# Kernel tuning notes

Measured on AMD Instinct MI355X. Metric: run time of the kernel, lower is better.

Reference implementation:

```python
import jax, jax.numpy as jnp
import numpy as np

N_USERS = 8192
D = 128
E = 262144        # known edges (nonzero_idx rows)
K = 131072        # static pad size for data-dependent candidate extraction
COS_THR = 0.3
TAU = 0.2


def setup_inputs() -> dict:
    key = jax.random.key(0)
    k1, k2, k3, k4 = jax.random.split(key, 4)
    user_emb = jax.random.normal(k1, (N_USERS, D), dtype=jnp.float32)
    nonzero_idx = jax.random.randint(k2, (E, 2), 0, N_USERS)
    W = jax.random.normal(k3, (2, 2 * D), dtype=jnp.float32) * 0.05  # mlp_s weight [2, 2*latent]
    b = jnp.zeros((2,), dtype=jnp.float32)                            # mlp_s bias
    gumbel_noise = jax.random.gumbel(k4, (E + K, 2), dtype=jnp.float32)
    return {"user_emb": user_emb, "W": W, "b": b,
            "gumbel_noise": gumbel_noise, "nonzero_idx": nonzero_idx}


def reference(user_emb, W, b, gumbel_noise, nonzero_idx):
    n = user_emb.shape[0]
    # ---- get_candidate_pair ----
    norm = jnp.linalg.norm(user_emb, axis=1, keepdims=True)
    u = user_emb / jnp.maximum(norm, 1e-12)          # F.normalize(dim=1)
    cos = u @ u.T                                    # [n, n]
    diag = jnp.arange(n)
    cos = cos.at[diag, diag].set(-1.0)               # fill_diagonal_(-1)
    cos = cos.at[nonzero_idx[:, 0], nonzero_idx[:, 1]].set(-1.0)
    mask = cos > COS_THR
    # static-size nonzero; padded slots point at (0,0) where cos == -1,
    # so they behave as invalid candidates (weight 0 downstream).
    ci, cj = jnp.nonzero(mask, size=K, fill_value=0)
    cand_vals = cos[ci, cj]                          # padded entries = -1
    cand_idx = jnp.stack([ci, cj], axis=1)           # [K, 2]

    # ---- forward ----
    pair_idx = jnp.concatenate([nonzero_idx, cand_idx], axis=0)   # [E+K, 2]
    u_emb = user_emb[pair_idx[:, 0]]
    v_emb = user_emb[pair_idx[:, 1]]
    concat_emb = jnp.concatenate([u_emb, v_emb], axis=1)          # [E+K, 2D]
    logits = concat_emb @ W.T + b                                 # [E+K, 2]

    # hard gumbel-softmax (straight-through)
    y_soft = jax.nn.softmax((logits + gumbel_noise) / TAU, axis=-1)
    y_hard = jax.nn.one_hot(jnp.argmax(y_soft, axis=-1), 2, dtype=y_soft.dtype)
    gumbel_output = y_hard + y_soft - jax.lax.stop_gradient(y_soft)
    gumbel_retain = gumbel_output[:, 0]                           # [E+K]

    # ---- get_edge_weight ----
    cand_w = jnp.maximum(cand_vals, 0.0)                          # masked_fill(<0, 0)
    weights = jnp.concatenate([jnp.ones((E,), dtype=cand_w.dtype), cand_w])
    w = gumbel_retain * weights                                   # [E+K]
    gumbel_01 = w
    gumbel_retain_w = jnp.concatenate([w[:, None], w[:, None]], axis=0)  # [2(E+K), 1]
    return gumbel_01, gumbel_retain_w, pair_idx
```

## Files before the change

kernel.cpp:

```cpp
#include <hip/hip_runtime.h>
#include <hip/hip_bf16.h>
#include <math.h>

#define N_USERS 8192
#define DIMS    128
#define EDGES   262144
#define KCAND   131072
#define NTOT    (EDGES + KCAND)
#define LISTCAP 131072
#define CAPB    512
#define NTILES  2080
#define COS_THR 0.3f
#define EPS_SEL 6e-3f
#define LOGIT_MARGIN 2e-3f
#define DEADKEY 0xFFFFFFFFu

typedef short bf16x8 __attribute__((ext_vector_type(8)));
typedef float f32x4  __attribute__((ext_vector_type(4)));


__global__ __launch_bounds__(256) void prep_k(const float* __restrict__ x,
                                              const float* __restrict__ W,
                                              const int* __restrict__ nz,
                                              float* __restrict__ un,
                                              unsigned short* __restrict__ u0,
                                              float4* __restrict__ P,
                                              unsigned* __restrict__ excl) {
  if (blockIdx.x < 32) {
#pragma clang fp contract(off)
    int i = blockIdx.x * 256 + threadIdx.x;
    const float* r = x + (size_t)i * DIMS;
    float a[8];
#pragma unroll
    for (int j = 0; j < 8; ++j) { float t = r[j]; a[j] = t * t; }
    for (int b8 = 8; b8 < DIMS; b8 += 8) {
#pragma unroll
      for (int j = 0; j < 8; ++j) { float t = r[b8 + j]; a[j] = a[j] + t * t; }
    }
    float s = ((a[0] + a[1]) + (a[2] + a[3])) + ((a[4] + a[5]) + (a[6] + a[7]));
    float n = (float)sqrt((double)s);
    n = fmaxf(n, 1e-12f);
    unsigned short* slab = u0 + (size_t)(i >> 7) * 16384 + (i & 127) * 8;
#pragma unroll
    for (int cq = 0; cq < 16; ++cq) {
      unsigned short tmp[8];
#pragma unroll
      for (int t = 0; t < 8; ++t) {
        float v = r[cq * 8 + t] / n;
        un[(size_t)i * DIMS + cq * 8 + t] = v;
        __hip_bfloat16 h = __float2bfloat16(v);
        tmp[t] = *(unsigned short*)&h;
      }
      *(uint4*)(slab + (size_t)cq * 1024) = *(uint4*)tmp;
    }
    float a0 = 0.f, b0 = 0.f, a1 = 0.f, b1 = 0.f;
    for (int k = 0; k < DIMS; ++k) {
      float t = r[k];
      a0 = fmaf(t, W[k], a0);
      b0 = fmaf(t, W[128 + k], b0);
      a1 = fmaf(t, W[256 + k], a1);
      b1 = fmaf(t, W[384 + k], b1);
    }
    P[i] = make_float4(a0, b0, a1, b1);
  } else {
    int t = (blockIdx.x - 32) * 256 + threadIdx.x;
    if (t < EDGES) {
      int i = nz[2 * t], j = nz[2 * t + 1];
      atomicOr(&excl[(size_t)i * 256 + (j >> 5)], 1u << (j & 31));
    }
  }
}

__global__ __launch_bounds__(512) void mfma_pass(const unsigned short* __restrict__ u0,
                                                 uint2* __restrict__ list,
                                                 int* __restrict__ gcount) {
  __shared__ __align__(16) unsigned short As[4][4][128][8];
  __shared__ __align__(16) unsigned short Bs[4][4][128][8];
  __shared__ uint2 svec[CAPB];
  __shared__ int lcnt, lbase;

  const int tid  = threadIdx.x;
  const int lane = tid & 63;
  const int wv   = tid >> 6;
  const int quad = lane >> 4;
  const int l15  = lane & 15;

  int rem = blockIdx.x, bi = 0;
  while (rem >= 64 - bi) { rem -= 64 - bi; ++bi; }
  const int bj = bi + rem;
  const int I0 = bi * 128, J0 = bj * 128;
  const int moff = (wv & 3) * 32, noff = (wv >> 2) * 64;

  if (tid == 0) lcnt = 0;

  const uint4* __restrict__ Aslab = (const uint4*)(u0 + (size_t)bi * 16384);
  const uint4* __restrict__ Bslab = (const uint4*)(u0 + (size_t)bj * 16384);
  uint4 pA[4], pB[4];
#pragma unroll
  for (int it = 0; it < 4; ++it) {
    pA[it] = Aslab[it * 512 + tid];
    pB[it] = Bslab[it * 512 + tid];
  }
#pragma unroll
  for (int it = 0; it < 4; ++it) {
    ((uint4*)As)[it * 512 + tid] = pA[it];
    ((uint4*)Bs)[it * 512 + tid] = pB[it];
  }
  __syncthreads();

  f32x4 acc[2][4];
#pragma unroll
  for (int mt = 0; mt < 2; ++mt)
#pragma unroll
    for (int nt = 0; nt < 4; ++nt)
#pragma unroll
      for (int g = 0; g < 4; ++g) acc[mt][nt][g] = 0.f;

#pragma unroll
  for (int kc = 0; kc < 4; ++kc) {
    bf16x8 af[2], bfr[4];
#pragma unroll
    for (int mt = 0; mt < 2; ++mt)
      af[mt] = *(const bf16x8*)&As[kc][quad][moff + mt * 16 + l15][0];
#pragma unroll
    for (int nt = 0; nt < 4; ++nt)
      bfr[nt] = *(const bf16x8*)&Bs[kc][quad][noff + nt * 16 + l15][0];
#pragma unroll
    for (int mt = 0; mt < 2; ++mt)
#pragma unroll
      for (int nt = 0; nt < 4; ++nt)
        acc[mt][nt] = __builtin_amdgcn_mfma_f32_16x16x32_bf16(
            af[mt], bfr[nt], acc[mt][nt], 0, 0, 0);
  }

#pragma unroll
  for (int mt = 0; mt < 2; ++mt)
#pragma unroll
    for (int nt = 0; nt < 4; ++nt)
#pragma unroll
      for (int g = 0; g < 4; ++g) {
        float v = acc[mt][nt][g];
        if (v > COS_THR - EPS_SEL) {
          int i = I0 + moff + mt * 16 + quad * 4 + g;
          int j = J0 + noff + nt * 16 + l15;
          if (j > i) {
            int idx = atomicAdd(&lcnt, 2);
            if (idx + 1 < CAPB) {
              svec[idx]     = make_uint2(((unsigned)i << 13) | j,
                                         __float_as_uint(v));
              svec[idx + 1] = make_uint2(((unsigned)j << 13) | i,
                                         __float_as_uint(v));
            }
          }
        }
      }

  __syncthreads();
  int n = min(lcnt, CAPB);
  if (tid == 0) lbase = atomicAdd(gcount, n);
  __syncthreads();
  int base = lbase;
  for (int t = tid; t < n; t += 512) {
    int o = base + t;
    if (o < LISTCAP) list[o] = svec[t];
  }
}

__global__ __launch_bounds__(256) void resolve_hist_k(const float* __restrict__ un,
                                                      const unsigned* __restrict__ excl,
                                                      uint2* __restrict__ list,
                                                      const int* __restrict__ gcount,
                                                      int* __restrict__ row_cnt) {
  int t = blockIdx.x * 256 + threadIdx.x;
  int n = min(*gcount, LISTCAP);
  if (t >= n) return;
  uint2 e = list[t];
  int i = e.x >> 13, j = e.x & 8191;
  unsigned word = excl[(size_t)i * 256 + (j >> 5)];
  bool alive = !(i == j || ((word >> (j & 31)) & 1u));
  float v = __uint_as_float(e.y);
  if (alive && v <= COS_THR + EPS_SEL) {
    const float* a = un + (size_t)i * DIMS;
    const float* b = un + (size_t)j * DIMS;
    float s = 0.f;
    for (int k = 0; k < DIMS; ++k) s = fmaf(a[k], b[k], s);
    alive = (s > COS_THR);
    if (alive) list[t] = make_uint2(e.x, __float_as_uint(s));
  }
  if (!alive) list[t] = make_uint2(DEADKEY, 0u);
  else        atomicAdd(&row_cnt[i], 1);
}

__global__ __launch_bounds__(256) void scan8k(const int* __restrict__ cnt,
                                              int* __restrict__ off) {
  __shared__ int sm[256];
  int t = threadIdx.x;
  int base = t * 32;
  int s = 0;
  for (int i = 0; i < 32; ++i) s += cnt[base + i];
  sm[t] = s;
  __syncthreads();
  int x = s;
  for (int d = 1; d < 256; d <<= 1) {
    int y = (t >= d) ? sm[t - d] : 0;
    __syncthreads();
    x += y;
    sm[t] = x;
    __syncthreads();
  }
  int run = x - s;
  for (int i = 0; i < 32; ++i) { off[base + i] = run; run += cnt[base + i]; }
  if (t == 255) off[N_USERS] = x;
}

__global__ __launch_bounds__(256) void scatter_pad_k(const uint2* __restrict__ list,
                                                     const int* __restrict__ gcount,
                                                     const int* __restrict__ row_off,
                                                     int* __restrict__ row_pos,
                                                     int* __restrict__ cand_i,
                                                     int* __restrict__ cand_j,
                                                     float* __restrict__ cand_v) {
  int t = blockIdx.x * 256 + threadIdx.x;
  int n = min(*gcount, LISTCAP);
  int M = row_off[N_USERS];
  if (t < n) {
    uint2 e = list[t];
    if (e.x != DEADKEY) {
      int i = e.x >> 13, j = e.x & 8191;
      int pos = row_off[i] + atomicAdd(&row_pos[i], 1);
      if (pos < KCAND) {
        cand_i[pos] = i;
        cand_j[pos] = j;
        cand_v[pos] = __uint_as_float(e.y);
      }
    }
  }
  if (t >= M && t < KCAND) { cand_i[t] = 0; cand_j[t] = 0; cand_v[t] = -1.0f; }
}

__global__ __launch_bounds__(256) void sortrow_k(const int* __restrict__ row_off,
                                                 const int* __restrict__ row_cnt,
                                                 int* __restrict__ cand_j,
                                                 float* __restrict__ cand_v) {
  int r = blockIdx.x * 256 + threadIdx.x;
  if (r >= N_USERS) return;
  int o = row_off[r], c = row_cnt[r];
  if (o + c > KCAND) c = max(0, KCAND - o);
  for (int a = 1; a < c; ++a) {
    int jv = cand_j[o + a];
    float vv = cand_v[o + a];
    int b = a - 1;
    while (b >= 0 && cand_j[o + b] > jv) {
      cand_j[o + b + 1] = cand_j[o + b];
      cand_v[o + b + 1] = cand_v[o + b];
      --b;
    }
    cand_j[o + b + 1] = jv;
    cand_v[o + b + 1] = vv;
  }
}

__global__ __launch_bounds__(256) void finalize_k(const float* __restrict__ ue,
                                                  const float* __restrict__ W,
                                                  const float* __restrict__ b,
                                                  const float* __restrict__ g,
                                                  const int* __restrict__ nz,
                                                  const int* __restrict__ cand_i,
                                                  const int* __restrict__ cand_j,
                                                  const float* __restrict__ cand_v,
                                                  const float4* __restrict__ P,
                                                  float* __restrict__ out) {
  int p = blockIdx.x * 256 + threadIdx.x;
  if (p >= NTOT) return;

  int i, j;
  float wgt;
  if (p < EDGES) {
    i = nz[2 * p];
    j = nz[2 * p + 1];
    wgt = 1.0f;
  } else {
    int q = p - EDGES;
    i = cand_i[q];
    j = cand_j[q];
    wgt = fmaxf(cand_v[q], 0.0f);
  }

  float4 Pi = P[i], Pj = P[j];
  float l0 = Pi.x + Pj.y + b[0];
  float l1 = Pi.z + Pj.w + b[1];
  float g0 = g[2 * p], g1 = g[2 * p + 1];
  float s0 = l0 + g0, s1 = l1 + g1;

  if (fabsf(s0 - s1) < LOGIT_MARGIN) {
    const float* ri = ue + (size_t)i * DIMS;
    const float* rj = ue + (size_t)j * DIMS;
    float e0 = 0.f, e1 = 0.f;
    for (int k = 0; k < DIMS; ++k) {
      e0 = fmaf(ri[k], W[k], e0);
      e1 = fmaf(ri[k], W[256 + k], e1);
    }
    for (int k = 0; k < DIMS; ++k) {
      e0 = fmaf(rj[k], W[128 + k], e0);
      e1 = fmaf(rj[k], W[384 + k], e1);
    }
    s0 = (e0 + b[0]) + g0;
    s1 = (e1 + b[1]) + g1;
  }

  float w = (s0 >= s1) ? wgt : 0.0f;

  out[p] = w;
  out[NTOT + p] = w;
  out[2 * NTOT + p] = w;
  out[3 * NTOT + 2 * p + 0] = (float)i;
  out[3 * NTOT + 2 * p + 1] = (float)j;
}

extern "C" void kernel_launch(void* const* d_in, const int* in_sizes, int n_in,
                              void* d_out, int out_size, void* d_ws, size_t ws_size,
                              hipStream_t stream) {
  (void)in_sizes; (void)n_in; (void)out_size; (void)ws_size;

  const float* user_emb = (const float*)d_in[0];
  const float* W        = (const float*)d_in[1];
  const float* b        = (const float*)d_in[2];
  const float* gnoise   = (const float*)d_in[3];
  const int*   nz       = (const int*)d_in[4];
  float* out = (float*)d_out;

  char* ws = (char*)d_ws;
  float*          un      = (float*)(ws + 0);
  unsigned short* u0      = (unsigned short*)(ws + (4u << 20));
  unsigned*       excl    = (unsigned*)(ws + (6u << 20));
  char*           zbase   = ws + (14u << 20);
  int*            gcount  = (int*)(zbase);
  int*            row_cnt = (int*)(zbase + 64);
  int*            row_pos = (int*)(zbase + 64 + 32768);
  int*            row_off = (int*)(ws + (14u << 20) + (96u << 10));
  uint2*          list    = (uint2*)(ws + (15u << 20));
  int*            cand_i  = (int*)(ws + (16u << 20));
  int*            cand_j  = (int*)(ws + (16u << 20) + (512u << 10));
  float*          cand_v  = (float*)(ws + (17u << 20));
  float4*         P       = (float4*)(ws + (17u << 20) + (512u << 10));

  hipMemsetAsync(excl, 0, (8u << 20) + (96u << 10), stream);

  prep_k<<<32 + EDGES / 256, 256, 0, stream>>>(user_emb, W, nz, un, u0, P, excl);
  mfma_pass<<<NTILES, 512, 0, stream>>>(u0, list, gcount);
  resolve_hist_k<<<LISTCAP / 256, 256, 0, stream>>>(un, excl, list, gcount,
                                                    row_cnt);
  scan8k<<<1, 256, 0, stream>>>(row_cnt, row_off);
  scatter_pad_k<<<KCAND / 256, 256, 0, stream>>>(list, gcount, row_off, row_pos,
                                                 cand_i, cand_j, cand_v);
  sortrow_k<<<N_USERS / 256, 256, 0, stream>>>(row_off, row_cnt, cand_j, cand_v);
  finalize_k<<<NTOT / 256, 256, 0, stream>>>(user_emb, W, b, gnoise, nz,
                                             cand_i, cand_j, cand_v, P, out);
}
```

Measured before the change: 162.2 us.

## Switch Gram tile to 32x32x16 MFMA, vectorize dot loops, move padding to finalize

The similarity tile kernel now runs 256 threads per block, each wave computing a 64x64 sub-tile with 32x32x16 bf16 MFMA instead of 16x16x32, and the LDS layout changes to match. The scalar dot products in resolve and finalize now use float4 loads with full unrolling. Padding-slot writes move out of the scatter kernel: finalize reads the candidate count and writes zero outputs directly for slots past it. The larger MFMA shape reduces LDS fragment loads per FLOP but needs more accumulator registers and changes the output index mapping, which the threshold/index code must follow exactly.

```diff
diff --git a/kernel.cpp b/kernel.cpp
--- a/kernel.cpp
+++ b/kernel.cpp
@@ -15,8 +15,8 @@
 #define LOGIT_MARGIN 2e-3f
 #define DEADKEY 0xFFFFFFFFu
 
-typedef short bf16x8 __attribute__((ext_vector_type(8)));
-typedef float f32x4  __attribute__((ext_vector_type(4)));
+typedef short bf16x8  __attribute__((ext_vector_type(8)));
+typedef float f32x16  __attribute__((ext_vector_type(16)));
 
 
 __global__ __launch_bounds__(256) void prep_k(const float* __restrict__ x,
@@ -71,78 +71,83 @@
   }
 }
 
-__global__ __launch_bounds__(512) void mfma_pass(const unsigned short* __restrict__ u0,
+__global__ __launch_bounds__(256) void mfma_pass(const unsigned short* __restrict__ u0,
                                                  uint2* __restrict__ list,
                                                  int* __restrict__ gcount) {
-  __shared__ __align__(16) unsigned short As[4][4][128][8];
-  __shared__ __align__(16) unsigned short Bs[4][4][128][8];
+  __shared__ __align__(16) unsigned short As[16][128][8];
+  __shared__ __align__(16) unsigned short Bs[16][128][8];
   __shared__ uint2 svec[CAPB];
   __shared__ int lcnt, lbase;
 
   const int tid  = threadIdx.x;
   const int lane = tid & 63;
   const int wv   = tid >> 6;
-  const int quad = lane >> 4;
-  const int l15  = lane & 15;
+  const int khalf = lane >> 5;
+  const int l31  = lane & 31;
 
   int rem = blockIdx.x, bi = 0;
   while (rem >= 64 - bi) { rem -= 64 - bi; ++bi; }
   const int bj = bi + rem;
   const int I0 = bi * 128, J0 = bj * 128;
-  const int moff = (wv & 3) * 32, noff = (wv >> 2) * 64;
+  const int moff = (wv & 1) * 64, noff = (wv >> 1) * 64;
 
   if (tid == 0) lcnt = 0;
 
   const uint4* __restrict__ Aslab = (const uint4*)(u0 + (size_t)bi * 16384);
   const uint4* __restrict__ Bslab = (const uint4*)(u0 + (size_t)bj * 16384);
-  uint4 pA[4], pB[4];
-#pragma unroll
-  for (int it = 0; it < 4; ++it) {
-    pA[it] = Aslab[it * 512 + tid];
-    pB[it] = Bslab[it * 512 + tid];
-  }
-#pragma unroll
-  for (int it = 0; it < 4; ++it) {
-    ((uint4*)As)[it * 512 + tid] = pA[it];
-    ((uint4*)Bs)[it * 512 + tid] = pB[it];
+#pragma unroll
+  for (int g = 0; g < 2; ++g) {
+    uint4 pa[4], pb[4];
+#pragma unroll
+    for (int it = 0; it < 4; ++it) {
+      int idx = (g * 4 + it) * 256 + tid;
+      pa[it] = Aslab[idx];
+      pb[it] = Bslab[idx];
+    }
+#pragma unroll
+    for (int it = 0; it < 4; ++it) {
+      int idx = (g * 4 + it) * 256 + tid;
+      ((uint4*)As)[idx] = pa[it];
+      ((uint4*)Bs)[idx] = pb[it];
+    }
   }
   __syncthreads();
 
-  f32x4 acc[2][4];
+  f32x16 acc[2][2];
 #pragma unroll
   for (int mt = 0; mt < 2; ++mt)
 #pragma unroll
-    for (int nt = 0; nt < 4; ++nt)
-#pragma unroll
-      for (int g = 0; g < 4; ++g) acc[mt][nt][g] = 0.f;
-
-#pragma unroll
-  for (int kc = 0; kc < 4; ++kc) {
-    bf16x8 af[2], bfr[4];
+    for (int nt = 0; nt < 2; ++nt)
+#pragma unroll
+      for (int g = 0; g < 16; ++g) acc[mt][nt][g] = 0.f;
+
+#pragma unroll
+  for (int kc = 0; kc < 8; ++kc) {
+    bf16x8 af[2], bf[2];
 #pragma unroll
     for (int mt = 0; mt < 2; ++mt)
-      af[mt] = *(const bf16x8*)&As[kc][quad][moff + mt * 16 + l15][0];
-#pragma unroll
-    for (int nt = 0; nt < 4; ++nt)
-      bfr[nt] = *(const bf16x8*)&Bs[kc][quad][noff + nt * 16 + l15][0];
+      af[mt] = *(const bf16x8*)&As[kc * 2 + khalf][moff + mt * 32 + l31][0];
+#pragma unroll
+    for (int nt = 0; nt < 2; ++nt)
+      bf[nt] = *(const bf16x8*)&Bs[kc * 2 + khalf][noff + nt * 32 + l31][0];
 #pragma unroll
     for (int mt = 0; mt < 2; ++mt)
 #pragma unroll
-      for (int nt = 0; nt < 4; ++nt)
-        acc[mt][nt] = __builtin_amdgcn_mfma_f32_16x16x32_bf16(
-            af[mt], bfr[nt], acc[mt][nt], 0, 0, 0);
+      for (int nt = 0; nt < 2; ++nt)
+        acc[mt][nt] = __builtin_amdgcn_mfma_f32_32x32x16_bf16(
+            af[mt], bf[nt], acc[mt][nt], 0, 0, 0);
   }
 
 #pragma unroll
   for (int mt = 0; mt < 2; ++mt)
 #pragma unroll
-    for (int nt = 0; nt < 4; ++nt)
-#pragma unroll
-      for (int g = 0; g < 4; ++g) {
-        float v = acc[mt][nt][g];
+    for (int nt = 0; nt < 2; ++nt)
+#pragma unroll
+      for (int r = 0; r < 16; ++r) {
+        float v = acc[mt][nt][r];
         if (v > COS_THR - EPS_SEL) {
-          int i = I0 + moff + mt * 16 + quad * 4 + g;
-          int j = J0 + noff + nt * 16 + l15;
+          int i = I0 + moff + mt * 32 + (r & 3) + 8 * (r >> 2) + 4 * khalf;
+          int j = J0 + noff + nt * 32 + l31;
           if (j > i) {
             int idx = atomicAdd(&lcnt, 2);
             if (idx + 1 < CAPB) {
@@ -160,7 +165,7 @@
   if (tid == 0) lbase = atomicAdd(gcount, n);
   __syncthreads();
   int base = lbase;
-  for (int t = tid; t < n; t += 512) {
+  for (int t = tid; t < n; t += 256) {
     int o = base + t;
     if (o < LISTCAP) list[o] = svec[t];
   }
@@ -180,10 +185,17 @@
   bool alive = !(i == j || ((word >> (j & 31)) & 1u));
   float v = __uint_as_float(e.y);
   if (alive && v <= COS_THR + EPS_SEL) {
-    const float* a = un + (size_t)i * DIMS;
-    const float* b = un + (size_t)j * DIMS;
+    const float4* a4 = (const float4*)(un + (size_t)i * DIMS);
+    const float4* b4 = (const float4*)(un + (size_t)j * DIMS);
     float s = 0.f;
-    for (int k = 0; k < DIMS; ++k) s = fmaf(a[k], b[k], s);
+#pragma unroll
+    for (int k4 = 0; k4 < 32; ++k4) {
+      float4 av = a4[k4], bv = b4[k4];
+      s = fmaf(av.x, bv.x, s);
+      s = fmaf(av.y, bv.y, s);
+      s = fmaf(av.z, bv.z, s);
+      s = fmaf(av.w, bv.w, s);
+    }
     alive = (s > COS_THR);
     if (alive) list[t] = make_uint2(e.x, __float_as_uint(s));
   }
@@ -213,29 +225,25 @@
   if (t == 255) off[N_USERS] = x;
 }
 
-__global__ __launch_bounds__(256) void scatter_pad_k(const uint2* __restrict__ list,
-                                                     const int* __restrict__ gcount,
-                                                     const int* __restrict__ row_off,
-                                                     int* __restrict__ row_pos,
-                                                     int* __restrict__ cand_i,
-                                                     int* __restrict__ cand_j,
-                                                     float* __restrict__ cand_v) {
+__global__ __launch_bounds__(256) void scatter_k(const uint2* __restrict__ list,
+                                                 const int* __restrict__ gcount,
+                                                 const int* __restrict__ row_off,
+                                                 int* __restrict__ row_pos,
+                                                 int* __restrict__ cand_i,
+                                                 int* __restrict__ cand_j,
+                                                 float* __restrict__ cand_v) {
   int t = blockIdx.x * 256 + threadIdx.x;
   int n = min(*gcount, LISTCAP);
-  int M = row_off[N_USERS];
-  if (t < n) {
-    uint2 e = list[t];
-    if (e.x != DEADKEY) {
-      int i = e.x >> 13, j = e.x & 8191;
-      int pos = row_off[i] + atomicAdd(&row_pos[i], 1);
-      if (pos < KCAND) {
-        cand_i[pos] = i;
-        cand_j[pos] = j;
-        cand_v[pos] = __uint_as_float(e.y);
-      }
-    }
-  }
-  if (t >= M && t < KCAND) { cand_i[t] = 0; cand_j[t] = 0; cand_v[t] = -1.0f; }
+  if (t >= n) return;
+  uint2 e = list[t];
+  if (e.x == DEADKEY) return;
+  int i = e.x >> 13, j = e.x & 8191;
+  int pos = row_off[i] + atomicAdd(&row_pos[i], 1);
+  if (pos < KCAND) {
+    cand_i[pos] = i;
+    cand_j[pos] = j;
+    cand_v[pos] = __uint_as_float(e.y);
+  }
 }
 
 __global__ __launch_bounds__(256) void sortrow_k(const int* __restrict__ row_off,
@@ -269,6 +277,7 @@
                                                   const int* __restrict__ cand_j,
                                                   const float* __restrict__ cand_v,
                                                   const float4* __restrict__ P,
+                                                  const int* __restrict__ gM,
                                                   float* __restrict__ out) {
   int p = blockIdx.x * 256 + threadIdx.x;
   if (p >= NTOT) return;
@@ -281,6 +290,14 @@
     wgt = 1.0f;
   } else {
     int q = p - EDGES;
+    if (q >= *gM) {
+      out[p] = 0.f;
+      out[NTOT + p] = 0.f;
+      out[2 * NTOT + p] = 0.f;
+      out[3 * NTOT + 2 * p + 0] = 0.f;
+      out[3 * NTOT + 2 * p + 1] = 0.f;
+      return;
+    }
     i = cand_i[q];
     j = cand_j[q];
     wgt = fmaxf(cand_v[q], 0.0f);
@@ -293,16 +310,32 @@
   float s0 = l0 + g0, s1 = l1 + g1;
 
   if (fabsf(s0 - s1) < LOGIT_MARGIN) {
-    const float* ri = ue + (size_t)i * DIMS;
-    const float* rj = ue + (size_t)j * DIMS;
+    const float4* ri = (const float4*)(ue + (size_t)i * DIMS);
+    const float4* rj = (const float4*)(ue + (size_t)j * DIMS);
     float e0 = 0.f, e1 = 0.f;
-    for (int k = 0; k < DIMS; ++k) {
-      e0 = fmaf(ri[k], W[k], e0);
-      e1 = fmaf(ri[k], W[256 + k], e1);
-    }
-    for (int k = 0; k < DIMS; ++k) {
-      e0 = fmaf(rj[k], W[128 + k], e0);
-      e1 = fmaf(rj[k], W[384 + k], e1);
+#pragma unroll
+    for (int k4 = 0; k4 < 32; ++k4) {
+      float4 av = ri[k4];
+      e0 = fmaf(av.x, W[k4 * 4 + 0], e0);
+      e0 = fmaf(av.y, W[k4 * 4 + 1], e0);
+      e0 = fmaf(av.z, W[k4 * 4 + 2], e0);
+      e0 = fmaf(av.w, W[k4 * 4 + 3], e0);
+      e1 = fmaf(av.x, W[256 + k4 * 4 + 0], e1);
+      e1 = fmaf(av.y, W[256 + k4 * 4 + 1], e1);
+      e1 = fmaf(av.z, W[256 + k4 * 4 + 2], e1);
+      e1 = fmaf(av.w, W[256 + k4 * 4 + 3], e1);
+    }
+#pragma unroll
+    for (int k4 = 0; k4 < 32; ++k4) {
+      float4 bv = rj[k4];
+      e0 = fmaf(bv.x, W[128 + k4 * 4 + 0], e0);
+      e0 = fmaf(bv.y, W[128 + k4 * 4 + 1], e0);
+      e0 = fmaf(bv.z, W[128 + k4 * 4 + 2], e0);
+      e0 = fmaf(bv.w, W[128 + k4 * 4 + 3], e0);
+      e1 = fmaf(bv.x, W[384 + k4 * 4 + 0], e1);
+      e1 = fmaf(bv.y, W[384 + k4 * 4 + 1], e1);
+      e1 = fmaf(bv.z, W[384 + k4 * 4 + 2], e1);
+      e1 = fmaf(bv.w, W[384 + k4 * 4 + 3], e1);
     }
     s0 = (e0 + b[0]) + g0;
     s1 = (e1 + b[1]) + g1;
@@ -347,13 +380,14 @@
   hipMemsetAsync(excl, 0, (8u << 20) + (96u << 10), stream);
 
   prep_k<<<32 + EDGES / 256, 256, 0, stream>>>(user_emb, W, nz, un, u0, P, excl);
-  mfma_pass<<<NTILES, 512, 0, stream>>>(u0, list, gcount);
+  mfma_pass<<<NTILES, 256, 0, stream>>>(u0, list, gcount);
   resolve_hist_k<<<LISTCAP / 256, 256, 0, stream>>>(un, excl, list, gcount,
                                                     row_cnt);
   scan8k<<<1, 256, 0, stream>>>(row_cnt, row_off);
-  scatter_pad_k<<<KCAND / 256, 256, 0, stream>>>(list, gcount, row_off, row_pos,
-                                                 cand_i, cand_j, cand_v);
+  scatter_k<<<LISTCAP / 256, 256, 0, stream>>>(list, gcount, row_off, row_pos,
+                                               cand_i, cand_j, cand_v);
   sortrow_k<<<N_USERS / 256, 256, 0, stream>>>(row_off, row_cnt, cand_j, cand_v);
   finalize_k<<<NTOT / 256, 256, 0, stream>>>(user_emb, W, b, gnoise, nz,
-                                             cand_i, cand_j, cand_v, P, out);
-}
+                                             cand_i, cand_j, cand_v, P,
+                                             row_off + N_USERS, out);
+}
```

New measurement: 164.8 us. About the same (+1.6%).
